# Kernel optimization log

Measured on AMD Instinct MI355X. Metric: run time of the kernel, lower is better.

Reference implementation:

```python
import jax, jax.numpy as jnp
import numpy as np

EPS = 1e-5
B, N = 16, 131072

def _bn(x, g, b, m, v):
    # x: [C, N]; inference-mode batchnorm with given stats
    return g[:, None] * (x - m[:, None]) * jax.lax.rsqrt(v[:, None] + EPS) + b[:, None]

def _make_npts():
    base = N // B
    offs = np.linspace(-2048, 2048, B).astype(np.int64)
    npts = np.full(B, base, dtype=np.int64) + offs
    npts[-1] += N - npts.sum()
    assert npts.sum() == N and (npts > 0).all()
    return npts

def setup_inputs() -> dict:
    key = jax.random.key(0)
    ks = jax.random.split(key, 16)
    d = {}
    d["x"] = jax.random.normal(ks[0], (3, N), jnp.float32)
    d["npts"] = jnp.asarray(_make_npts(), jnp.int32)
    def w(k, o, i):
        return jax.random.normal(k, (o, i), jnp.float32) * (1.0 / np.sqrt(i))
    def bnp(k, c):
        k1, k2, k3, k4 = jax.random.split(k, 4)
        return (1.0 + 0.1 * jax.random.normal(k1, (c,), jnp.float32),
                0.1 * jax.random.normal(k2, (c,), jnp.float32),
                0.1 * jax.random.normal(k3, (c,), jnp.float32),
                0.5 + jax.random.uniform(k4, (c,), jnp.float32))
    d["W1"] = w(ks[1], 128, 3);   d["b1"] = jnp.zeros(128, jnp.float32)
    d["g1"], d["be1"], d["m1"], d["v1"] = bnp(ks[2], 128)
    d["W2"] = w(ks[3], 256, 128); d["b2"] = jnp.zeros(256, jnp.float32)
    d["g2"], d["be2"], d["m2"], d["v2"] = bnp(ks[4], 256)
    d["W3"] = w(ks[5], 512, 512); d["b3"] = jnp.zeros(512, jnp.float32)
    d["g3"], d["be3"], d["m3"], d["v3"] = bnp(ks[6], 512)
    d["W4"] = w(ks[7], 1024, 512); d["b4"] = jnp.zeros(1024, jnp.float32)
    d["g4"], d["be4"], d["m4"], d["v4"] = bnp(ks[8], 1024)
    return d

def reference(x, npts,
              W1, b1, g1, be1, m1, v1,
              W2, b2, g2, be2, m2, v2,
              W3, b3, g3, be3, m3, v3,
              W4, b4, g4, be4, m4, v4):
    # segment ids for the ragged point->cloud mapping (replaces torch.split loops)
    seg = jnp.repeat(jnp.arange(B, dtype=jnp.int32), npts, total_repeat_length=N)  # [N]
    h = jax.nn.relu(_bn(W1 @ x + b1[:, None], g1, be1, m1, v1))        # [128, N]
    f = _bn(W2 @ h + b2[:, None], g2, be2, m2, v2)                      # [256, N]
    g = jax.ops.segment_max(f.T, seg, num_segments=B)                   # [B, 256]
    gs = g[seg].T                                                       # [256, N] broadcast back
    xc = jnp.concatenate([gs, f], axis=0)                               # [512, N]
    h3 = jax.nn.relu(_bn(W3 @ xc + b3[:, None], g3, be3, m3, v3))       # [512, N]
    h4 = _bn(W4 @ h3 + b4[:, None], g4, be4, m4, v4)                    # [1024, N]
    v = jax.ops.segment_max(h4.T, seg, num_segments=B)                  # [B, 1024]
    return v
```

## Files before the change

### kernel.cpp

```cpp
#include <hip/hip_runtime.h>
#include <hip/hip_bf16.h>
#include <stdint.h>

#define NTOT 131072
#define NSEG 16
#define EPSV 1e-5f

typedef __attribute__((ext_vector_type(8))) short bf16x8;
typedef __attribute__((ext_vector_type(4))) float f32x4;

struct Args {
  const float* x; const int* npts;
  const float *W1,*b1,*g1,*be1,*m1,*v1;
  const float *W2,*b2,*g2,*be2,*m2,*v2;
  const float *W3,*b3,*g3,*be3,*m3,*v3;
  const float *W4,*b4,*g4,*be4,*m4,*v4;
  int* offs;
  float *a1,*c1,*a2,*c2,*a3,*c3,*a4,*c4;
  unsigned int *gkeys,*vkeys;
  unsigned short *w2b;
  unsigned short *w3p;
  unsigned short *w4p;
  unsigned short *fbufp;
  unsigned short *h3p;
  float* cseg;
  float* out;
};

__device__ inline unsigned int f2key(float f){ unsigned u=__float_as_uint(f); return (u&0x80000000u)? ~u : (u|0x80000000u); }
__device__ inline float key2f(unsigned k){ unsigned u=(k&0x80000000u)? (k^0x80000000u) : ~k; return __uint_as_float(u); }
__device__ inline unsigned short f2bf(float f){ __hip_bfloat16 h=__float2bfloat16(f); return *(unsigned short*)&h; }

__device__ inline void gl16(const void* g, void* l){
  __builtin_amdgcn_global_load_lds((const __attribute__((address_space(1))) unsigned int*)g,
                                   (__attribute__((address_space(3))) unsigned int*)l, 16, 0, 0);
}

__global__ void k_setup(Args A){
  int tid = threadIdx.x;
  if (tid==0){ int s=0; A.offs[0]=0; for (int i=0;i<NSEG;i++){ s+=A.npts[i]; A.offs[i+1]=s; } }
  for (int c=tid;c<128;c+=256){ float a=A.g1[c]*rsqrtf(A.v1[c]+EPSV); A.a1[c]=a; A.c1[c]=A.be1[c]+a*(A.b1[c]-A.m1[c]); }
  for (int c=tid;c<256;c+=256){ float a=A.g2[c]*rsqrtf(A.v2[c]+EPSV); A.a2[c]=a; A.c2[c]=A.be2[c]+a*(A.b2[c]-A.m2[c]); }
  for (int c=tid;c<512;c+=256){ float a=A.g3[c]*rsqrtf(A.v3[c]+EPSV); A.a3[c]=a; A.c3[c]=A.be3[c]+a*(A.b3[c]-A.m3[c]); }
  for (int c=tid;c<1024;c+=256){ float a=A.g4[c]*rsqrtf(A.v4[c]+EPSV); A.a4[c]=a; A.c4[c]=A.be4[c]+a*(A.b4[c]-A.m4[c]); }
  for (int i=tid;i<NSEG*256;i+=256)  A.gkeys[i]=0u;
  for (int i=tid;i<NSEG*1024;i+=256) A.vkeys[i]=0u;
}

__global__ void k_conv(Args A){
  const int n1=256*128;
  const int n2=131072;
  const int n3=524288;
  for (int i = blockIdx.x*256+threadIdx.x; i < n1+n2+n3; i += gridDim.x*256){
    if (i<n1) A.w2b[i]=f2bf(A.W2[i]);
    else if (i<n1+n2){
      int o=i-n1; int j=o&7, cr=(o>>3)&127, kgg=(o>>10)&31, mt=o>>15;
      A.w3p[o]=f2bf(A.W3[(size_t)(mt*128+cr)*512 + 256 + kgg*8 + j]);
    } else {
      int o=i-n1-n2; int j=o&7, cr=(o>>3)&127, kgg=(o>>10)&63, mt=o>>16;
      A.w4p[o]=f2bf(A.W4[(size_t)(mt*128+cr)*512 + kgg*8 + j]);
    }
  }
}

__global__ __launch_bounds__(256) void k_l12(Args A){
  __shared__ float w1s[384], a1s[128], c1s[128], a2s[256], c2s[256];
  __shared__ float xs[3][64];
  __shared__ int offs_s[NSEG+1], segp[64];
  __shared__ unsigned short hs[16*64*8];
  int tid=threadIdx.x, pt0=blockIdx.x*64;
  for (int i=tid;i<384;i+=256) w1s[i]=A.W1[i];
  if (tid<128){ a1s[tid]=A.a1[tid]; c1s[tid]=A.c1[tid]; }
  a2s[tid]=A.a2[tid]; c2s[tid]=A.c2[tid];
  if (tid<=NSEG) offs_s[tid]=A.offs[tid];
  if (tid<64){ xs[0][tid]=A.x[pt0+tid]; xs[1][tid]=A.x[NTOT+pt0+tid]; xs[2][tid]=A.x[2*NTOT+pt0+tid]; }
  __syncthreads();
  if (tid<64){ int gp=pt0+tid, s=0; while (gp>=offs_s[s+1]) s++; segp[tid]=s; }
  for (int pair=tid; pair<1024; pair+=256){
    int pt=pair&63, kc=pair>>6;
    float x0=xs[0][pt], x1=xs[1][pt], x2=xs[2][pt];
    unsigned short us[8];
    #pragma unroll
    for (int j=0;j<8;j++){
      int cin=kc*8+j;
      float v = fmaf(w1s[cin*3],x0, fmaf(w1s[cin*3+1],x1, w1s[cin*3+2]*x2));
      v = fmaxf(fmaf(a1s[cin],v,c1s[cin]), 0.f);
      us[j]=f2bf(v);
    }
    uint4 pk;
    pk.x=(unsigned)us[0]|((unsigned)us[1]<<16); pk.y=(unsigned)us[2]|((unsigned)us[3]<<16);
    pk.z=(unsigned)us[4]|((unsigned)us[5]<<16); pk.w=(unsigned)us[6]|((unsigned)us[7]<<16);
    *(uint4*)(&hs[(kc*64+pt)*8]) = pk;
  }
  __syncthreads();
  int lane=tid&63, wv=tid>>6, quad=lane>>4, l16=lane&15;
  int m0=wv*64;
  f32x4 acc[4][4];
  for (int a=0;a<4;a++)
    for (int b=0;b<4;b++)
      acc[a][b]=(f32x4){0.f,0.f,0.f,0.f};
  #pragma unroll
  for (int ks=0; ks<4; ++ks){
    bf16x8 bfr[4];
    #pragma unroll
    for (int nt=0; nt<4; ++nt) bfr[nt]=*(bf16x8*)(&hs[((ks*4+quad)*64 + nt*16 + l16)*8]);
    #pragma unroll
    for (int mt=0; mt<4; ++mt){
      bf16x8 afr = *(const bf16x8*)(&A.w2b[(m0+mt*16+l16)*128 + ks*32 + quad*8]);
      #pragma unroll
      for (int nt=0; nt<4; ++nt)
        acc[mt][nt]=__builtin_amdgcn_mfma_f32_16x16x32_bf16(afr, bfr[nt], acc[mt][nt], 0,0,0);
    }
  }
  bool uni = (segp[0]==segp[63]); int seg0=segp[0];
  size_t tb = (size_t)(blockIdx.x>>1)*32768;
  int prelb = (blockIdx.x&1)*64;
  #pragma unroll
  for (int mt=0;mt<4;++mt){
    int cout0=m0+mt*16+quad*4;
    int kg=cout0>>3, sub=cout0&7;
    float fv[4][4];
    #pragma unroll
    for (int nt=0;nt<4;++nt)
      #pragma unroll
      for (int r=0;r<4;++r)
        fv[nt][r]=fmaf(a2s[cout0+r], acc[mt][nt][r], c2s[cout0+r]);
    #pragma unroll
    for (int nt=0;nt<4;++nt){
      int ptl=nt*16+l16;
      uint2 pk;
      pk.x=(unsigned)f2bf(fv[nt][0])|((unsigned)f2bf(fv[nt][1])<<16);
      pk.y=(unsigned)f2bf(fv[nt][2])|((unsigned)f2bf(fv[nt][3])<<16);
      *(uint2*)&A.fbufp[tb + (size_t)((kg*128 + prelb + ptl)*8 + sub)] = pk;
    }
    #pragma unroll
    for (int r=0;r<4;++r){
      if (uni){
        float mv=fmaxf(fmaxf(fv[0][r],fv[1][r]),fmaxf(fv[2][r],fv[3][r]));
        #pragma unroll
        for (int off=8;off>=1;off>>=1) mv=fmaxf(mv, __shfl_xor(mv,off));
        if (l16==0) atomicMax(&A.gkeys[seg0*256+cout0+r], f2key(mv));
      } else {
        #pragma unroll
        for (int nt=0;nt<4;++nt)
          atomicMax(&A.gkeys[segp[nt*16+l16]*256+cout0+r], f2key(fv[nt][r]));
      }
    }
  }
}

__global__ void k_cseg(Args A){
  int seg = blockIdx.x>>1; int cout = (blockIdx.x&1)*256 + threadIdx.x;
  __shared__ float gs[256];
  gs[threadIdx.x] = key2f(A.gkeys[seg*256+threadIdx.x]);
  __syncthreads();
  const float* wrow = A.W3 + (size_t)cout*512;
  float s=0.f;
  #pragma unroll 8
  for (int k=0;k<256;k++) s = fmaf(wrow[k], gs[k], s);
  A.cseg[seg*512+cout]=s;
}

__global__ __launch_bounds__(256,4) void k_l3(Args A){
  __shared__ unsigned short sA[8192], sB[8192];
  __shared__ int offs_s[NSEG+1];
  int bid=blockIdx.x, xcd=bid&7, idx=bid>>3;
  int mtile=idx&3, ntile=xcd*128+(idx>>2);
  int tid=threadIdx.x, lane=tid&63, wv=tid>>6, quad=lane>>4, l16=lane&15;
  int mq=wv&1, nq=wv>>1;
  const char* wbase=(const char*)A.w3p   + (size_t)mtile*65536;
  const char* bbase=(const char*)A.fbufp + (size_t)ntile*65536;
  if (tid<=NSEG) offs_s[tid]=A.offs[tid];
  f32x4 acc[4][4];
  for (int a=0;a<4;a++)
    for (int b=0;b<4;b++)
      acc[a][b]=(f32x4){0.f,0.f,0.f,0.f};
  for (int s=0;s<4;++s){
    const char* srcA = wbase + s*16384;
    const char* srcB = bbase + s*16384;
    #pragma unroll
    for (int i=0;i<4;++i){
      gl16(srcA + wv*4096 + i*1024 + lane*16, (char*)sA + wv*4096 + i*1024);
      gl16(srcB + wv*4096 + i*1024 + lane*16, (char*)sB + wv*4096 + i*1024);
    }
    __syncthreads();
    #pragma unroll
    for (int ks=0;ks<2;++ks){
      bf16x8 bb[4], afr[4];
      #pragma unroll
      for (int nt=0;nt<4;++nt) bb[nt]=*(const bf16x8*)(&sB[((ks*4+quad)*128 + nq*64 + nt*16 + l16)*8]);
      #pragma unroll
      for (int mt=0;mt<4;++mt) afr[mt]=*(const bf16x8*)(&sA[((ks*4+quad)*128 + mq*64 + mt*16 + l16)*8]);
      #pragma unroll
      for (int mt=0;mt<4;++mt)
        #pragma unroll
        for (int nt=0;nt<4;++nt)
          acc[mt][nt]=__builtin_amdgcn_mfma_f32_16x16x32_bf16(afr[mt], bb[nt], acc[mt][nt], 0,0,0);
    }
    __syncthreads();
  }
  int pt0 = ntile*128 + nq*64;
  int sBeg=0; while (pt0 >= offs_s[sBeg+1]) sBeg++;
  int sEnd=sBeg; while (pt0+63 >= offs_s[sEnd+1]) sEnd++;
  bool uni=(sBeg==sEnd);
  int segl[4];
  if (!uni){
    #pragma unroll
    for (int nt=0;nt<4;++nt){ int gp=pt0+nt*16+l16, ss=sBeg; while (gp>=offs_s[ss+1]) ss++; segl[nt]=ss; }
  }
  size_t hb = (size_t)ntile*65536;
  #pragma unroll
  for (int mt=0;mt<4;++mt){
    int cout0=mtile*128 + mq*64 + mt*16 + quad*4;
    int kg=cout0>>3, sub=cout0&7;
    float sa[4],sc[4],csr[4];
    #pragma unroll
    for (int r=0;r<4;++r){ sa[r]=A.a3[cout0+r]; sc[r]=A.c3[cout0+r]; }
    if (uni){
      #pragma unroll
      for (int r=0;r<4;++r) csr[r]=A.cseg[sBeg*512+cout0+r];
    }
    #pragma unroll
    for (int nt=0;nt<4;++nt){
      int prel=nq*64+nt*16+l16;
      unsigned short us[4];
      #pragma unroll
      for (int r=0;r<4;++r){
        float cv = uni? csr[r] : A.cseg[segl[nt]*512+cout0+r];
        float hv = fmaxf(fmaf(sa[r], acc[mt][nt][r]+cv, sc[r]), 0.f);
        us[r]=f2bf(hv);
      }
      uint2 pk;
      pk.x=(unsigned)us[0]|((unsigned)us[1]<<16);
      pk.y=(unsigned)us[2]|((unsigned)us[3]<<16);
      *(uint2*)&A.h3p[hb + (size_t)((kg*128+prel)*8+sub)] = pk;
    }
  }
}

__global__ __launch_bounds__(256,4) void k_l4(Args A){
  __shared__ unsigned short sA[8192], sB[8192];
  __shared__ int offs_s[NSEG+1];
  int bid=blockIdx.x, xcd=bid&7, idx=bid>>3;
  int mtile=idx&7, ntile=xcd*128+(idx>>3);
  int tid=threadIdx.x, lane=tid&63, wv=tid>>6, quad=lane>>4, l16=lane&15;
  int mq=wv&1, nq=wv>>1;
  const char* wbase=(const char*)A.w4p + (size_t)mtile*131072;
  const char* bbase=(const char*)A.h3p + (size_t)ntile*131072;
  if (tid<=NSEG) offs_s[tid]=A.offs[tid];
  f32x4 acc[4][4];
  for (int a=0;a<4;a++)
    for (int b=0;b<4;b++)
      acc[a][b]=(f32x4){0.f,0.f,0.f,0.f};
  for (int s=0;s<8;++s){
    const char* srcA = wbase + s*16384;
    const char* srcB = bbase + s*16384;
    #pragma unroll
    for (int i=0;i<4;++i){
      gl16(srcA + wv*4096 + i*1024 + lane*16, (char*)sA + wv*4096 + i*1024);
      gl16(srcB + wv*4096 + i*1024 + lane*16, (char*)sB + wv*4096 + i*1024);
    }
    __syncthreads();
    #pragma unroll
    for (int ks=0;ks<2;++ks){
      bf16x8 bb[4], afr[4];
      #pragma unroll
      for (int nt=0;nt<4;++nt) bb[nt]=*(const bf16x8*)(&sB[((ks*4+quad)*128 + nq*64 + nt*16 + l16)*8]);
      #pragma unroll
      for (int mt=0;mt<4;++mt) afr[mt]=*(const bf16x8*)(&sA[((ks*4+quad)*128 + mq*64 + mt*16 + l16)*8]);
      #pragma unroll
      for (int mt=0;mt<4;++mt)
        #pragma unroll
        for (int nt=0;nt<4;++nt)
          acc[mt][nt]=__builtin_amdgcn_mfma_f32_16x16x32_bf16(afr[mt], bb[nt], acc[mt][nt], 0,0,0);
    }
    __syncthreads();
  }
  int pt0 = ntile*128 + nq*64;
  int sBeg=0; while (pt0 >= offs_s[sBeg+1]) sBeg++;
  int sEnd=sBeg; while (pt0+63 >= offs_s[sEnd+1]) sEnd++;
  bool uni=(sBeg==sEnd);
  int segl[4];
  if (!uni){
    #pragma unroll
    for (int nt=0;nt<4;++nt){ int gp=pt0+nt*16+l16, ss=sBeg; while (gp>=offs_s[ss+1]) ss++; segl[nt]=ss; }
  }
  #pragma unroll
  for (int mt=0;mt<4;++mt){
    int cout0=mtile*128 + mq*64 + mt*16 + quad*4;
    #pragma unroll
    for (int r=0;r<4;++r){
      int cout=cout0+r;
      float sa=A.a4[cout], sc=A.c4[cout];
      float mv=-3.4e38f;
      #pragma unroll
      for (int nt=0;nt<4;++nt){
        float fv=fmaf(sa, acc[mt][nt][r], sc);
        if (uni) mv=fmaxf(mv,fv);
        else atomicMax(&A.vkeys[segl[nt]*1024+cout], f2key(fv));
      }
      if (uni){
        #pragma unroll
        for (int off=8;off>=1;off>>=1) mv=fmaxf(mv, __shfl_xor(mv,off));
        if (l16==0) atomicMax(&A.vkeys[sBeg*1024+cout], f2key(mv));
      }
    }
  }
}

__global__ void k_final(Args A){
  int i=blockIdx.x*256+threadIdx.x;
  if (i<NSEG*1024) A.out[i]=key2f(A.vkeys[i]);
}

extern "C" void kernel_launch(void* const* d_in, const int* in_sizes, int n_in,
                              void* d_out, int out_size, void* d_ws, size_t ws_size,
                              hipStream_t stream){
  Args A;
  A.x  =(const float*)d_in[0];  A.npts=(const int*)d_in[1];
  A.W1 =(const float*)d_in[2];  A.b1 =(const float*)d_in[3];
  A.g1 =(const float*)d_in[4];  A.be1=(const float*)d_in[5];
  A.m1 =(const float*)d_in[6];  A.v1 =(const float*)d_in[7];
  A.W2 =(const float*)d_in[8];  A.b2 =(const float*)d_in[9];
  A.g2 =(const float*)d_in[10]; A.be2=(const float*)d_in[11];
  A.m2 =(const float*)d_in[12]; A.v2 =(const float*)d_in[13];
  A.W3 =(const float*)d_in[14]; A.b3 =(const float*)d_in[15];
  A.g3 =(const float*)d_in[16]; A.be3=(const float*)d_in[17];
  A.m3 =(const float*)d_in[18]; A.v3 =(const float*)d_in[19];
  A.W4 =(const float*)d_in[20]; A.b4 =(const float*)d_in[21];
  A.g4 =(const float*)d_in[22]; A.be4=(const float*)d_in[23];
  A.m4 =(const float*)d_in[24]; A.v4 =(const float*)d_in[25];

  char* w=(char*)d_ws;
  auto alloc=[&](size_t b)->void*{ void* p=(void*)w; w += (b+255)&~(size_t)255; return p; };
  A.offs =(int*)alloc((NSEG+1)*4);
  A.a1=(float*)alloc(128*4);  A.c1=(float*)alloc(128*4);
  A.a2=(float*)alloc(256*4);  A.c2=(float*)alloc(256*4);
  A.a3=(float*)alloc(512*4);  A.c3=(float*)alloc(512*4);
  A.a4=(float*)alloc(1024*4); A.c4=(float*)alloc(1024*4);
  A.gkeys=(unsigned int*)alloc(NSEG*256*4);
  A.vkeys=(unsigned int*)alloc(NSEG*1024*4);
  A.cseg =(float*)alloc(NSEG*512*4);
  A.w2b=(unsigned short*)alloc(256*128*2);
  A.w3p=(unsigned short*)alloc(131072*2);
  A.w4p=(unsigned short*)alloc(524288*2);
  A.fbufp=(unsigned short*)alloc((size_t)1024*32768*2);
  A.h3p  =(unsigned short*)alloc((size_t)1024*65536*2);
  A.out=(float*)d_out;

  k_setup<<<dim3(1),dim3(256),0,stream>>>(A);
  k_conv <<<dim3(2688),dim3(256),0,stream>>>(A);
  k_l12  <<<dim3(NTOT/64),dim3(256),0,stream>>>(A);
  k_cseg <<<dim3(32),dim3(256),0,stream>>>(A);
  k_l3   <<<dim3(4096),dim3(256),0,stream>>>(A);
  k_l4   <<<dim3(8192),dim3(256),0,stream>>>(A);
  k_final<<<dim3(64),dim3(256),0,stream>>>(A);
}
```

Measured before the change: 604.2 us.

## Double-buffer LDS and make L3/L4 GEMM blocks persistent over four N-tiles

```diff
diff --git a/kernel.cpp b/kernel.cpp
--- a/kernel.cpp
+++ b/kernel.cpp
@@ -161,150 +161,192 @@
   A.cseg[seg*512+cout]=s;
 }
 
-__global__ __launch_bounds__(256,4) void k_l3(Args A){
-  __shared__ unsigned short sA[8192], sB[8192];
+__global__ __launch_bounds__(256,2) void k_l3(Args A){
+  __shared__ unsigned short sA[2][8192], sB[2][8192];
   __shared__ int offs_s[NSEG+1];
+  const int NST=16;
   int bid=blockIdx.x, xcd=bid&7, idx=bid>>3;
-  int mtile=idx&3, ntile=xcd*128+(idx>>2);
+  int mtile=idx&3, nq4=idx>>2;
+  int nbase=(xcd*32+nq4)*4;
   int tid=threadIdx.x, lane=tid&63, wv=tid>>6, quad=lane>>4, l16=lane&15;
   int mq=wv&1, nq=wv>>1;
-  const char* wbase=(const char*)A.w3p   + (size_t)mtile*65536;
-  const char* bbase=(const char*)A.fbufp + (size_t)ntile*65536;
+  const char* wbase=(const char*)A.w3p + (size_t)mtile*65536;
+  const char* bbase0=(const char*)A.fbufp;
   if (tid<=NSEG) offs_s[tid]=A.offs[tid];
   f32x4 acc[4][4];
   for (int a=0;a<4;a++)
     for (int b=0;b<4;b++)
       acc[a][b]=(f32x4){0.f,0.f,0.f,0.f};
-  for (int s=0;s<4;++s){
+
+  auto stage=[&](int buf,int ntile,int s){
     const char* srcA = wbase + s*16384;
-    const char* srcB = bbase + s*16384;
-    #pragma unroll
-    for (int i=0;i<4;++i){
-      gl16(srcA + wv*4096 + i*1024 + lane*16, (char*)sA + wv*4096 + i*1024);
-      gl16(srcB + wv*4096 + i*1024 + lane*16, (char*)sB + wv*4096 + i*1024);
+    const char* srcB = bbase0 + (size_t)ntile*65536 + s*16384;
+    char* dA=(char*)&sA[buf][0]; char* dB=(char*)&sB[buf][0];
+    #pragma unroll
+    for(int i=0;i<4;++i){
+      gl16(srcA + wv*4096 + i*1024 + lane*16, dA + wv*4096 + i*1024);
+      gl16(srcB + wv*4096 + i*1024 + lane*16, dB + wv*4096 + i*1024);
+    }
+  };
+
+  stage(0, nbase, 0);
+  __syncthreads();
+  for (int g=0; g<NST; ++g){
+    int buf=g&1, ntile=nbase+(g>>2), s=g&3;
+    bf16x8 afr[2][4], bbv[2][4];
+    #pragma unroll
+    for (int ks=0;ks<2;++ks){
+      #pragma unroll
+      for (int mt=0;mt<4;++mt) afr[ks][mt]=*(const bf16x8*)(&sA[buf][((ks*4+quad)*128 + mq*64 + mt*16 + l16)*8]);
+      #pragma unroll
+      for (int nt=0;nt<4;++nt) bbv[ks][nt]=*(const bf16x8*)(&sB[buf][((ks*4+quad)*128 + nq*64 + nt*16 + l16)*8]);
+    }
+    __builtin_amdgcn_sched_barrier(0);
+    if (g+1<NST) stage((g+1)&1, nbase+((g+1)>>2), (g+1)&3);
+    __builtin_amdgcn_sched_barrier(0);
+    __builtin_amdgcn_s_setprio(1);
+    #pragma unroll
+    for (int ks=0;ks<2;++ks)
+      #pragma unroll
+      for (int mt=0;mt<4;++mt)
+        #pragma unroll
+        for (int nt=0;nt<4;++nt)
+          acc[mt][nt]=__builtin_amdgcn_mfma_f32_16x16x32_bf16(afr[ks][mt], bbv[ks][nt], acc[mt][nt], 0,0,0);
+    __builtin_amdgcn_s_setprio(0);
+    if (s==3){
+      int pt0 = ntile*128 + nq*64;
+      int sBeg=0; while (pt0 >= offs_s[sBeg+1]) sBeg++;
+      int sEnd=sBeg; while (pt0+63 >= offs_s[sEnd+1]) sEnd++;
+      bool uni=(sBeg==sEnd);
+      int segl[4];
+      if (!uni){
+        #pragma unroll
+        for (int nt=0;nt<4;++nt){ int gp=pt0+nt*16+l16, ss=sBeg; while (gp>=offs_s[ss+1]) ss++; segl[nt]=ss; }
+      }
+      size_t hb = (size_t)ntile*65536;
+      #pragma unroll
+      for (int mt=0;mt<4;++mt){
+        int cout0=mtile*128 + mq*64 + mt*16 + quad*4;
+        int kg=cout0>>3, sub=cout0&7;
+        float sa[4],sc[4],csr[4];
+        #pragma unroll
+        for (int r=0;r<4;++r){ sa[r]=A.a3[cout0+r]; sc[r]=A.c3[cout0+r]; }
+        if (uni){
+          #pragma unroll
+          for (int r=0;r<4;++r) csr[r]=A.cseg[sBeg*512+cout0+r];
+        }
+        #pragma unroll
+        for (int nt=0;nt<4;++nt){
+          int prel=nq*64+nt*16+l16;
+          unsigned short us[4];
+          #pragma unroll
+          for (int r=0;r<4;++r){
+            float cv = uni? csr[r] : A.cseg[segl[nt]*512+cout0+r];
+            float hv = fmaxf(fmaf(sa[r], acc[mt][nt][r]+cv, sc[r]), 0.f);
+            us[r]=f2bf(hv);
+          }
+          uint2 pk;
+          pk.x=(unsigned)us[0]|((unsigned)us[1]<<16);
+          pk.y=(unsigned)us[2]|((unsigned)us[3]<<16);
+          *(uint2*)&A.h3p[hb + (size_t)((kg*128+prel)*8+sub)] = pk;
+        }
+      }
+      for (int a=0;a<4;a++)
+        for (int b=0;b<4;b++)
+          acc[a][b]=(f32x4){0.f,0.f,0.f,0.f};
     }
     __syncthreads();
-    #pragma unroll
-    for (int ks=0;ks<2;++ks){
-      bf16x8 bb[4], afr[4];
-      #pragma unroll
-      for (int nt=0;nt<4;++nt) bb[nt]=*(const bf16x8*)(&sB[((ks*4+quad)*128 + nq*64 + nt*16 + l16)*8]);
-      #pragma unroll
-      for (int mt=0;mt<4;++mt) afr[mt]=*(const bf16x8*)(&sA[((ks*4+quad)*128 + mq*64 + mt*16 + l16)*8]);
-      #pragma unroll
-      for (int mt=0;mt<4;++mt)
-        #pragma unroll
-        for (int nt=0;nt<4;++nt)
-          acc[mt][nt]=__builtin_amdgcn_mfma_f32_16x16x32_bf16(afr[mt], bb[nt], acc[mt][nt], 0,0,0);
-    }
-    __syncthreads();
-  }
-  int pt0 = ntile*128 + nq*64;
-  int sBeg=0; while (pt0 >= offs_s[sBeg+1]) sBeg++;
-  int sEnd=sBeg; while (pt0+63 >= offs_s[sEnd+1]) sEnd++;
-  bool uni=(sBeg==sEnd);
-  int segl[4];
-  if (!uni){
-    #pragma unroll
-    for (int nt=0;nt<4;++nt){ int gp=pt0+nt*16+l16, ss=sBeg; while (gp>=offs_s[ss+1]) ss++; segl[nt]=ss; }
-  }
-  size_t hb = (size_t)ntile*65536;
-  #pragma unroll
-  for (int mt=0;mt<4;++mt){
-    int cout0=mtile*128 + mq*64 + mt*16 + quad*4;
-    int kg=cout0>>3, sub=cout0&7;
-    float sa[4],sc[4],csr[4];
-    #pragma unroll
-    for (int r=0;r<4;++r){ sa[r]=A.a3[cout0+r]; sc[r]=A.c3[cout0+r]; }
-    if (uni){
-      #pragma unroll
-      for (int r=0;r<4;++r) csr[r]=A.cseg[sBeg*512+cout0+r];
-    }
-    #pragma unroll
-    for (int nt=0;nt<4;++nt){
-      int prel=nq*64+nt*16+l16;
-      unsigned short us[4];
-      #pragma unroll
-      for (int r=0;r<4;++r){
-        float cv = uni? csr[r] : A.cseg[segl[nt]*512+cout0+r];
-        float hv = fmaxf(fmaf(sa[r], acc[mt][nt][r]+cv, sc[r]), 0.f);
-        us[r]=f2bf(hv);
-      }
-      uint2 pk;
-      pk.x=(unsigned)us[0]|((unsigned)us[1]<<16);
-      pk.y=(unsigned)us[2]|((unsigned)us[3]<<16);
-      *(uint2*)&A.h3p[hb + (size_t)((kg*128+prel)*8+sub)] = pk;
-    }
-  }
-}
-
-__global__ __launch_bounds__(256,4) void k_l4(Args A){
-  __shared__ unsigned short sA[8192], sB[8192];
+  }
+}
+
+__global__ __launch_bounds__(256,2) void k_l4(Args A){
+  __shared__ unsigned short sA[2][8192], sB[2][8192];
   __shared__ int offs_s[NSEG+1];
+  const int NST=32;
   int bid=blockIdx.x, xcd=bid&7, idx=bid>>3;
-  int mtile=idx&7, ntile=xcd*128+(idx>>3);
+  int mtile=idx&7, nq4=idx>>3;
+  int nbase=(xcd*32+nq4)*4;
   int tid=threadIdx.x, lane=tid&63, wv=tid>>6, quad=lane>>4, l16=lane&15;
   int mq=wv&1, nq=wv>>1;
   const char* wbase=(const char*)A.w4p + (size_t)mtile*131072;
-  const char* bbase=(const char*)A.h3p + (size_t)ntile*131072;
+  const char* bbase0=(const char*)A.h3p;
   if (tid<=NSEG) offs_s[tid]=A.offs[tid];
   f32x4 acc[4][4];
   for (int a=0;a<4;a++)
     for (int b=0;b<4;b++)
       acc[a][b]=(f32x4){0.f,0.f,0.f,0.f};
-  for (int s=0;s<8;++s){
+
+  auto stage=[&](int buf,int ntile,int s){
     const char* srcA = wbase + s*16384;
-    const char* srcB = bbase + s*16384;
-    #pragma unroll
-    for (int i=0;i<4;++i){
-      gl16(srcA + wv*4096 + i*1024 + lane*16, (char*)sA + wv*4096 + i*1024);
-      gl16(srcB + wv*4096 + i*1024 + lane*16, (char*)sB + wv*4096 + i*1024);
+    const char* srcB = bbase0 + (size_t)ntile*131072 + s*16384;
+    char* dA=(char*)&sA[buf][0]; char* dB=(char*)&sB[buf][0];
+    #pragma unroll
+    for(int i=0;i<4;++i){
+      gl16(srcA + wv*4096 + i*1024 + lane*16, dA + wv*4096 + i*1024);
+      gl16(srcB + wv*4096 + i*1024 + lane*16, dB + wv*4096 + i*1024);
+    }
+  };
+
+  stage(0, nbase, 0);
+  __syncthreads();
+  for (int g=0; g<NST; ++g){
+    int buf=g&1, ntile=nbase+(g>>3), s=g&7;
+    bf16x8 afr[2][4], bbv[2][4];
+    #pragma unroll
+    for (int ks=0;ks<2;++ks){
+      #pragma unroll
+      for (int mt=0;mt<4;++mt) afr[ks][mt]=*(const bf16x8*)(&sA[buf][((ks*4+quad)*128 + mq*64 + mt*16 + l16)*8]);
+      #pragma unroll
+      for (int nt=0;nt<4;++nt) bbv[ks][nt]=*(const bf16x8*)(&sB[buf][((ks*4+quad)*128 + nq*64 + nt*16 + l16)*8]);
+    }
+    __builtin_amdgcn_sched_barrier(0);
+    if (g+1<NST) stage((g+1)&1, nbase+((g+1)>>3), (g+1)&7);
+    __builtin_amdgcn_sched_barrier(0);
+    __builtin_amdgcn_s_setprio(1);
+    #pragma unroll
+    for (int ks=0;ks<2;++ks)
+      #pragma unroll
+      for (int mt=0;mt<4;++mt)
+        #pragma unroll
+        for (int nt=0;nt<4;++nt)
+          acc[mt][nt]=__builtin_amdgcn_mfma_f32_16x16x32_bf16(afr[ks][mt], bbv[ks][nt], acc[mt][nt], 0,0,0);
+    __builtin_amdgcn_s_setprio(0);
+    if (s==7){
+      int pt0 = ntile*128 + nq*64;
+      int sBeg=0; while (pt0 >= offs_s[sBeg+1]) sBeg++;
+      int sEnd=sBeg; while (pt0+63 >= offs_s[sEnd+1]) sEnd++;
+      bool uni=(sBeg==sEnd);
+      int segl[4];
+      if (!uni){
+        #pragma unroll
+        for (int nt=0;nt<4;++nt){ int gp=pt0+nt*16+l16, ss=sBeg; while (gp>=offs_s[ss+1]) ss++; segl[nt]=ss; }
+      }
+      #pragma unroll
+      for (int mt=0;mt<4;++mt){
+        int cout0=mtile*128 + mq*64 + mt*16 + quad*4;
+        #pragma unroll
+        for (int r=0;r<4;++r){
+          int cout=cout0+r;
+          float sa=A.a4[cout], sc=A.c4[cout];
+          float mv=-3.4e38f;
+          #pragma unroll
+          for (int nt=0;nt<4;++nt){
+            float fv=fmaf(sa, acc[mt][nt][r], sc);
+            if (uni) mv=fmaxf(mv,fv);
+            else atomicMax(&A.vkeys[segl[nt]*1024+cout], f2key(fv));
+          }
+          if (uni){
+            #pragma unroll
+            for (int off=8;off>=1;off>>=1) mv=fmaxf(mv, __shfl_xor(mv,off));
+            if (l16==0) atomicMax(&A.vkeys[sBeg*1024+cout], f2key(mv));
+          }
+        }
+      }
+      for (int a=0;a<4;a++)
+        for (int b=0;b<4;b++)
+          acc[a][b]=(f32x4){0.f,0.f,0.f,0.f};
     }
     __syncthreads();
-    #pragma unroll
-    for (int ks=0;ks<2;++ks){
-      bf16x8 bb[4], afr[4];
-      #pragma unroll
-      for (int nt=0;nt<4;++nt) bb[nt]=*(const bf16x8*)(&sB[((ks*4+quad)*128 + nq*64 + nt*16 + l16)*8]);
-      #pragma unroll
-      for (int mt=0;mt<4;++mt) afr[mt]=*(const bf16x8*)(&sA[((ks*4+quad)*128 + mq*64 + mt*16 + l16)*8]);
-      #pragma unroll
-      for (int mt=0;mt<4;++mt)
-        #pragma unroll
-        for (int nt=0;nt<4;++nt)
-          acc[mt][nt]=__builtin_amdgcn_mfma_f32_16x16x32_bf16(afr[mt], bb[nt], acc[mt][nt], 0,0,0);
-    }
-    __syncthreads();
-  }
-  int pt0 = ntile*128 + nq*64;
-  int sBeg=0; while (pt0 >= offs_s[sBeg+1]) sBeg++;
-  int sEnd=sBeg; while (pt0+63 >= offs_s[sEnd+1]) sEnd++;
-  bool uni=(sBeg==sEnd);
-  int segl[4];
-  if (!uni){
-    #pragma unroll
-    for (int nt=0;nt<4;++nt){ int gp=pt0+nt*16+l16, ss=sBeg; while (gp>=offs_s[ss+1]) ss++; segl[nt]=ss; }
-  }
-  #pragma unroll
-  for (int mt=0;mt<4;++mt){
-    int cout0=mtile*128 + mq*64 + mt*16 + quad*4;
-    #pragma unroll
-    for (int r=0;r<4;++r){
-      int cout=cout0+r;
-      float sa=A.a4[cout], sc=A.c4[cout];
-      float mv=-3.4e38f;
-      #pragma unroll
-      for (int nt=0;nt<4;++nt){
-        float fv=fmaf(sa, acc[mt][nt][r], sc);
-        if (uni) mv=fmaxf(mv,fv);
-        else atomicMax(&A.vkeys[segl[nt]*1024+cout], f2key(fv));
-      }
-      if (uni){
-        #pragma unroll
-        for (int off=8;off>=1;off>>=1) mv=fmaxf(mv, __shfl_xor(mv,off));
-        if (l16==0) atomicMax(&A.vkeys[sBeg*1024+cout], f2key(mv));
-      }
-    }
   }
 }
 
@@ -352,7 +394,7 @@
   k_conv <<<dim3(2688),dim3(256),0,stream>>>(A);
   k_l12  <<<dim3(NTOT/64),dim3(256),0,stream>>>(A);
   k_cseg <<<dim3(32),dim3(256),0,stream>>>(A);
-  k_l3   <<<dim3(4096),dim3(256),0,stream>>>(A);
-  k_l4   <<<dim3(8192),dim3(256),0,stream>>>(A);
+  k_l3   <<<dim3(1024),dim3(256),0,stream>>>(A);
+  k_l4   <<<dim3(2048),dim3(256),0,stream>>>(A);
   k_final<<<dim3(64),dim3(256),0,stream>>>(A);
 }
```

After: 726.8 us. 20.3% more time.

## Fuse layer-3 and layer-4 GEMMs into one kernel keeping h3 in LDS

Applied to the files above, without the earlier changes.

```diff
diff --git a/kernel.cpp b/kernel.cpp
--- a/kernel.cpp
+++ b/kernel.cpp
@@ -22,7 +22,6 @@
   unsigned short *w3p;
   unsigned short *w4p;
   unsigned short *fbufp;
-  unsigned short *h3p;
   float* cseg;
   float* out;
 };
@@ -54,11 +53,11 @@
   for (int i = blockIdx.x*256+threadIdx.x; i < n1+n2+n3; i += gridDim.x*256){
     if (i<n1) A.w2b[i]=f2bf(A.W2[i]);
     else if (i<n1+n2){
-      int o=i-n1; int j=o&7, cr=(o>>3)&127, kgg=(o>>10)&31, mt=o>>15;
-      A.w3p[o]=f2bf(A.W3[(size_t)(mt*128+cr)*512 + 256 + kgg*8 + j]);
+      int o=i-n1; int j=o&7, cout=(o>>3)&255, kgrel=(o>>11)&3, ks=(o>>13)&7, cg=(o>>16)&1;
+      A.w3p[o]=f2bf(A.W3[(size_t)(cg*256+cout)*512 + 256 + ks*32 + kgrel*8 + j]);
     } else {
-      int o=i-n1-n2; int j=o&7, cr=(o>>3)&127, kgg=(o>>10)&63, mt=o>>16;
-      A.w4p[o]=f2bf(A.W4[(size_t)(mt*128+cr)*512 + kgg*8 + j]);
+      int o=i-n1-n2; int j=o&7, cout=(o>>3)&255, kgrel=(o>>11)&3, ks=(o>>13)&15, cg=(o>>17)&3;
+      A.w4p[o]=f2bf(A.W4[(size_t)(cg*256+cout)*512 + ks*32 + kgrel*8 + j]);
     }
   }
 }
@@ -113,8 +112,6 @@
     }
   }
   bool uni = (segp[0]==segp[63]); int seg0=segp[0];
-  size_t tb = (size_t)(blockIdx.x>>1)*32768;
-  int prelb = (blockIdx.x&1)*64;
   #pragma unroll
   for (int mt=0;mt<4;++mt){
     int cout0=m0+mt*16+quad*4;
@@ -131,7 +128,8 @@
       uint2 pk;
       pk.x=(unsigned)f2bf(fv[nt][0])|((unsigned)f2bf(fv[nt][1])<<16);
       pk.y=(unsigned)f2bf(fv[nt][2])|((unsigned)f2bf(fv[nt][3])<<16);
-      *(uint2*)&A.fbufp[tb + (size_t)((kg*128 + prelb + ptl)*8 + sub)] = pk;
+      size_t o = (size_t)(blockIdx.x*2 + (nt>>1))*8192 + (size_t)(kg*256 + ((nt&1)*16+l16)*8 + sub);
+      *(uint2*)&A.fbufp[o] = pk;
     }
     #pragma unroll
     for (int r=0;r<4;++r){
@@ -161,148 +159,157 @@
   A.cseg[seg*512+cout]=s;
 }
 
-__global__ __launch_bounds__(256,4) void k_l3(Args A){
-  __shared__ unsigned short sA[8192], sB[8192];
+__global__ __launch_bounds__(512,1) void k_l34(Args A){
+  __shared__ unsigned short h3s[65536];
+  __shared__ unsigned short fstg[8192];
   __shared__ int offs_s[NSEG+1];
-  int bid=blockIdx.x, xcd=bid&7, idx=bid>>3;
-  int mtile=idx&3, ntile=xcd*128+(idx>>2);
+  int blk=blockIdx.x;
   int tid=threadIdx.x, lane=tid&63, wv=tid>>6, quad=lane>>4, l16=lane&15;
-  int mq=wv&1, nq=wv>>1;
-  const char* wbase=(const char*)A.w3p   + (size_t)mtile*65536;
-  const char* bbase=(const char*)A.fbufp + (size_t)ntile*65536;
   if (tid<=NSEG) offs_s[tid]=A.offs[tid];
-  f32x4 acc[4][4];
-  for (int a=0;a<4;a++)
-    for (int b=0;b<4;b++)
-      acc[a][b]=(f32x4){0.f,0.f,0.f,0.f};
-  for (int s=0;s<4;++s){
-    const char* srcA = wbase + s*16384;
-    const char* srcB = bbase + s*16384;
-    #pragma unroll
-    for (int i=0;i<4;++i){
-      gl16(srcA + wv*4096 + i*1024 + lane*16, (char*)sA + wv*4096 + i*1024);
-      gl16(srcB + wv*4096 + i*1024 + lane*16, (char*)sB + wv*4096 + i*1024);
-    }
+  int c0=wv*64;
+
+  for (int chunk=0;chunk<4;++chunk){
+    const char* src=(const char*)A.fbufp + ((size_t)(blk*4+chunk))*16384;
+    gl16(src + wv*2048 + lane*16, (char*)fstg + wv*2048);
+    gl16(src + wv*2048 + 1024 + lane*16, (char*)fstg + wv*2048 + 1024);
     __syncthreads();
-    #pragma unroll
-    for (int ks=0;ks<2;++ks){
-      bf16x8 bb[4], afr[4];
-      #pragma unroll
-      for (int nt=0;nt<4;++nt) bb[nt]=*(const bf16x8*)(&sB[((ks*4+quad)*128 + nq*64 + nt*16 + l16)*8]);
-      #pragma unroll
-      for (int mt=0;mt<4;++mt) afr[mt]=*(const bf16x8*)(&sA[((ks*4+quad)*128 + mq*64 + mt*16 + l16)*8]);
+    f32x4 acc1[4][2];
+    #pragma unroll
+    for (int mt=0;mt<4;++mt)
+      #pragma unroll
+      for (int nt=0;nt<2;++nt)
+        acc1[mt][nt]=(f32x4){0.f,0.f,0.f,0.f};
+    #pragma unroll
+    for (int kk=0;kk<8;++kk){
+      bf16x8 bfr[2], afr[4];
+      #pragma unroll
+      for (int nt=0;nt<2;++nt)
+        bfr[nt]=*(const bf16x8*)(&fstg[((kk*4+quad)*32 + nt*16 + l16)*8]);
+      #pragma unroll
+      for (int mt=0;mt<4;++mt){
+        int cout=c0+mt*16+l16;
+        afr[mt]=*(const bf16x8*)(A.w3p + (size_t)((cout>>8)*65536 + kk*8192 + quad*2048 + (cout&255)*8));
+      }
+      __builtin_amdgcn_s_setprio(1);
       #pragma unroll
       for (int mt=0;mt<4;++mt)
         #pragma unroll
+        for (int nt=0;nt<2;++nt)
+          acc1[mt][nt]=__builtin_amdgcn_mfma_f32_16x16x32_bf16(afr[mt], bfr[nt], acc1[mt][nt], 0,0,0);
+      __builtin_amdgcn_s_setprio(0);
+    }
+    int pt0c = blk*128 + chunk*32;
+    int sBeg=0; while (pt0c >= offs_s[sBeg+1]) sBeg++;
+    int sEnd=sBeg; while (pt0c+31 >= offs_s[sEnd+1]) sEnd++;
+    bool uni=(sBeg==sEnd);
+    int segl[2];
+    if (!uni){
+      #pragma unroll
+      for (int nt=0;nt<2;++nt){ int gp=pt0c+nt*16+l16, ss=sBeg; while (gp>=offs_s[ss+1]) ss++; segl[nt]=ss; }
+    }
+    #pragma unroll
+    for (int mt=0;mt<4;++mt){
+      int cout0=c0+mt*16+quad*4;
+      int kg3=cout0>>3, sub3=cout0&7;
+      float sa[4],sc[4],csr[4];
+      #pragma unroll
+      for (int r=0;r<4;++r){ sa[r]=A.a3[cout0+r]; sc[r]=A.c3[cout0+r]; }
+      if (uni){
+        #pragma unroll
+        for (int r=0;r<4;++r) csr[r]=A.cseg[sBeg*512+cout0+r];
+      }
+      #pragma unroll
+      for (int nt=0;nt<2;++nt){
+        int ptt=chunk*32+nt*16+l16;
+        unsigned short us[4];
+        #pragma unroll
+        for (int r=0;r<4;++r){
+          float cv = uni? csr[r] : A.cseg[segl[nt]*512+cout0+r];
+          float hv = fmaxf(fmaf(sa[r], acc1[mt][nt][r]+cv, sc[r]), 0.f);
+          us[r]=f2bf(hv);
+        }
+        uint2 pk;
+        pk.x=(unsigned)us[0]|((unsigned)us[1]<<16);
+        pk.y=(unsigned)us[2]|((unsigned)us[3]<<16);
+        *(uint2*)&h3s[(size_t)((kg3*128+ptt)*8+sub3)] = pk;
+      }
+    }
+    __syncthreads();
+  }
+
+  for (int ci=0;ci<2;++ci){
+    int cc0=ci*512+c0;
+    f32x4 acc2[2][4][4];
+    #pragma unroll
+    for (int pi=0;pi<2;++pi)
+      #pragma unroll
+      for (int mt=0;mt<4;++mt)
+        #pragma unroll
         for (int nt=0;nt<4;++nt)
-          acc[mt][nt]=__builtin_amdgcn_mfma_f32_16x16x32_bf16(afr[mt], bb[nt], acc[mt][nt], 0,0,0);
-    }
-    __syncthreads();
-  }
-  int pt0 = ntile*128 + nq*64;
-  int sBeg=0; while (pt0 >= offs_s[sBeg+1]) sBeg++;
-  int sEnd=sBeg; while (pt0+63 >= offs_s[sEnd+1]) sEnd++;
-  bool uni=(sBeg==sEnd);
-  int segl[4];
-  if (!uni){
-    #pragma unroll
-    for (int nt=0;nt<4;++nt){ int gp=pt0+nt*16+l16, ss=sBeg; while (gp>=offs_s[ss+1]) ss++; segl[nt]=ss; }
-  }
-  size_t hb = (size_t)ntile*65536;
-  #pragma unroll
-  for (int mt=0;mt<4;++mt){
-    int cout0=mtile*128 + mq*64 + mt*16 + quad*4;
-    int kg=cout0>>3, sub=cout0&7;
-    float sa[4],sc[4],csr[4];
-    #pragma unroll
-    for (int r=0;r<4;++r){ sa[r]=A.a3[cout0+r]; sc[r]=A.c3[cout0+r]; }
-    if (uni){
-      #pragma unroll
-      for (int r=0;r<4;++r) csr[r]=A.cseg[sBeg*512+cout0+r];
-    }
-    #pragma unroll
-    for (int nt=0;nt<4;++nt){
-      int prel=nq*64+nt*16+l16;
-      unsigned short us[4];
-      #pragma unroll
-      for (int r=0;r<4;++r){
-        float cv = uni? csr[r] : A.cseg[segl[nt]*512+cout0+r];
-        float hv = fmaxf(fmaf(sa[r], acc[mt][nt][r]+cv, sc[r]), 0.f);
-        us[r]=f2bf(hv);
-      }
-      uint2 pk;
-      pk.x=(unsigned)us[0]|((unsigned)us[1]<<16);
-      pk.y=(unsigned)us[2]|((unsigned)us[3]<<16);
-      *(uint2*)&A.h3p[hb + (size_t)((kg*128+prel)*8+sub)] = pk;
-    }
-  }
-}
-
-__global__ __launch_bounds__(256,4) void k_l4(Args A){
-  __shared__ unsigned short sA[8192], sB[8192];
-  __shared__ int offs_s[NSEG+1];
-  int bid=blockIdx.x, xcd=bid&7, idx=bid>>3;
-  int mtile=idx&7, ntile=xcd*128+(idx>>3);
-  int tid=threadIdx.x, lane=tid&63, wv=tid>>6, quad=lane>>4, l16=lane&15;
-  int mq=wv&1, nq=wv>>1;
-  const char* wbase=(const char*)A.w4p + (size_t)mtile*131072;
-  const char* bbase=(const char*)A.h3p + (size_t)ntile*131072;
-  if (tid<=NSEG) offs_s[tid]=A.offs[tid];
-  f32x4 acc[4][4];
-  for (int a=0;a<4;a++)
-    for (int b=0;b<4;b++)
-      acc[a][b]=(f32x4){0.f,0.f,0.f,0.f};
-  for (int s=0;s<8;++s){
-    const char* srcA = wbase + s*16384;
-    const char* srcB = bbase + s*16384;
-    #pragma unroll
-    for (int i=0;i<4;++i){
-      gl16(srcA + wv*4096 + i*1024 + lane*16, (char*)sA + wv*4096 + i*1024);
-      gl16(srcB + wv*4096 + i*1024 + lane*16, (char*)sB + wv*4096 + i*1024);
-    }
-    __syncthreads();
-    #pragma unroll
-    for (int ks=0;ks<2;++ks){
-      bf16x8 bb[4], afr[4];
-      #pragma unroll
-      for (int nt=0;nt<4;++nt) bb[nt]=*(const bf16x8*)(&sB[((ks*4+quad)*128 + nq*64 + nt*16 + l16)*8]);
-      #pragma unroll
-      for (int mt=0;mt<4;++mt) afr[mt]=*(const bf16x8*)(&sA[((ks*4+quad)*128 + mq*64 + mt*16 + l16)*8]);
-      #pragma unroll
-      for (int mt=0;mt<4;++mt)
+          acc2[pi][mt][nt]=(f32x4){0.f,0.f,0.f,0.f};
+    bf16x8 aF[2][4];
+    #pragma unroll
+    for (int mt=0;mt<4;++mt){
+      int cout=cc0+mt*16+l16;
+      aF[0][mt]=*(const bf16x8*)(A.w4p + (size_t)((cout>>8)*131072 + quad*2048 + (cout&255)*8));
+    }
+    #pragma unroll
+    for (int kk=0;kk<16;++kk){
+      const int cb=kk&1, nb=cb^1;
+      if (kk<15){
+        #pragma unroll
+        for (int mt=0;mt<4;++mt){
+          int cout=cc0+mt*16+l16;
+          aF[nb][mt]=*(const bf16x8*)(A.w4p + (size_t)((cout>>8)*131072 + (kk+1)*8192 + quad*2048 + (cout&255)*8));
+        }
+      }
+      bf16x8 b2[2][4];
+      #pragma unroll
+      for (int pi=0;pi<2;++pi)
         #pragma unroll
         for (int nt=0;nt<4;++nt)
-          acc[mt][nt]=__builtin_amdgcn_mfma_f32_16x16x32_bf16(afr[mt], bb[nt], acc[mt][nt], 0,0,0);
-    }
-    __syncthreads();
-  }
-  int pt0 = ntile*128 + nq*64;
-  int sBeg=0; while (pt0 >= offs_s[sBeg+1]) sBeg++;
-  int sEnd=sBeg; while (pt0+63 >= offs_s[sEnd+1]) sEnd++;
-  bool uni=(sBeg==sEnd);
-  int segl[4];
-  if (!uni){
-    #pragma unroll
-    for (int nt=0;nt<4;++nt){ int gp=pt0+nt*16+l16, ss=sBeg; while (gp>=offs_s[ss+1]) ss++; segl[nt]=ss; }
-  }
-  #pragma unroll
-  for (int mt=0;mt<4;++mt){
-    int cout0=mtile*128 + mq*64 + mt*16 + quad*4;
-    #pragma unroll
-    for (int r=0;r<4;++r){
-      int cout=cout0+r;
-      float sa=A.a4[cout], sc=A.c4[cout];
-      float mv=-3.4e38f;
-      #pragma unroll
-      for (int nt=0;nt<4;++nt){
-        float fv=fmaf(sa, acc[mt][nt][r], sc);
-        if (uni) mv=fmaxf(mv,fv);
-        else atomicMax(&A.vkeys[segl[nt]*1024+cout], f2key(fv));
-      }
-      if (uni){
-        #pragma unroll
-        for (int off=8;off>=1;off>>=1) mv=fmaxf(mv, __shfl_xor(mv,off));
-        if (l16==0) atomicMax(&A.vkeys[sBeg*1024+cout], f2key(mv));
+          b2[pi][nt]=*(const bf16x8*)(&h3s[(size_t)(((kk*4+quad)*128 + pi*64 + nt*16 + l16)*8)]);
+      __builtin_amdgcn_s_setprio(1);
+      #pragma unroll
+      for (int pi=0;pi<2;++pi)
+        #pragma unroll
+        for (int mt=0;mt<4;++mt)
+          #pragma unroll
+          for (int nt=0;nt<4;++nt)
+            acc2[pi][mt][nt]=__builtin_amdgcn_mfma_f32_16x16x32_bf16(aF[cb][mt], b2[pi][nt], acc2[pi][mt][nt], 0,0,0);
+      __builtin_amdgcn_s_setprio(0);
+    }
+    #pragma unroll
+    for (int pi=0;pi<2;++pi){
+      int pt0=blk*128+pi*64;
+      int sBeg=0; while (pt0 >= offs_s[sBeg+1]) sBeg++;
+      int sEnd=sBeg; while (pt0+63 >= offs_s[sEnd+1]) sEnd++;
+      bool uni=(sBeg==sEnd);
+      int segl[4];
+      if (!uni){
+        #pragma unroll
+        for (int nt=0;nt<4;++nt){ int gp=pt0+nt*16+l16, ss=sBeg; while (gp>=offs_s[ss+1]) ss++; segl[nt]=ss; }
+      }
+      #pragma unroll
+      for (int mt=0;mt<4;++mt){
+        int cout0=cc0+mt*16+quad*4;
+        #pragma unroll
+        for (int r=0;r<4;++r){
+          int cout=cout0+r;
+          float sa=A.a4[cout], sc=A.c4[cout];
+          float mv=-3.4e38f;
+          #pragma unroll
+          for (int nt=0;nt<4;++nt){
+            float fv=fmaf(sa, acc2[pi][mt][nt][r], sc);
+            if (uni) mv=fmaxf(mv,fv);
+            else atomicMax(&A.vkeys[segl[nt]*1024+cout], f2key(fv));
+          }
+          if (uni){
+            #pragma unroll
+            for (int off=8;off>=1;off>>=1) mv=fmaxf(mv, __shfl_xor(mv,off));
+            if (l16==0) atomicMax(&A.vkeys[sBeg*1024+cout], f2key(mv));
+          }
+        }
       }
     }
   }
@@ -344,15 +351,13 @@
   A.w2b=(unsigned short*)alloc(256*128*2);
   A.w3p=(unsigned short*)alloc(131072*2);
   A.w4p=(unsigned short*)alloc(524288*2);
-  A.fbufp=(unsigned short*)alloc((size_t)1024*32768*2);
-  A.h3p  =(unsigned short*)alloc((size_t)1024*65536*2);
+  A.fbufp=(unsigned short*)alloc((size_t)4096*8192*2);
   A.out=(float*)d_out;
 
   k_setup<<<dim3(1),dim3(256),0,stream>>>(A);
   k_conv <<<dim3(2688),dim3(256),0,stream>>>(A);
   k_l12  <<<dim3(NTOT/64),dim3(256),0,stream>>>(A);
   k_cseg <<<dim3(32),dim3(256),0,stream>>>(A);
-  k_l3   <<<dim3(4096),dim3(256),0,stream>>>(A);
-  k_l4   <<<dim3(8192),dim3(256),0,stream>>>(A);
+  k_l34  <<<dim3(1024),dim3(512),0,stream>>>(A);
   k_final<<<dim3(64),dim3(256),0,stream>>>(A);
 }
```

Measured after the change: 933.3 us. 1.54x slower.

## Retile L3/L4 GEMMs to 256x64 blocks with weight fragments read directly from global

Applied to the files above, without the earlier changes.

```diff
diff --git a/kernel.cpp b/kernel.cpp
--- a/kernel.cpp
+++ b/kernel.cpp
@@ -162,35 +162,34 @@
 }
 
 __global__ __launch_bounds__(256,4) void k_l3(Args A){
-  __shared__ unsigned short sA[8192], sB[8192];
+  __shared__ unsigned short sB[4096];
   __shared__ int offs_s[NSEG+1];
-  int bid=blockIdx.x, xcd=bid&7, idx=bid>>3;
-  int mtile=idx&3, ntile=xcd*128+(idx>>2);
+  int bid=blockIdx.x, xcd=bid&7, j=bid>>3;
+  int Mt=j&1, ntile=xcd+8*(j>>1);
   int tid=threadIdx.x, lane=tid&63, wv=tid>>6, quad=lane>>4, l16=lane&15;
-  int mq=wv&1, nq=wv>>1;
-  const char* wbase=(const char*)A.w3p   + (size_t)mtile*65536;
-  const char* bbase=(const char*)A.fbufp + (size_t)ntile*65536;
+  int half=ntile&1, nt128=ntile>>1;
+  const char* bbase=(const char*)A.fbufp + (size_t)nt128*65536 + half*1024;
   if (tid<=NSEG) offs_s[tid]=A.offs[tid];
+  int coutw = Mt*256 + wv*64;
   f32x4 acc[4][4];
   for (int a=0;a<4;a++)
     for (int b=0;b<4;b++)
       acc[a][b]=(f32x4){0.f,0.f,0.f,0.f};
   for (int s=0;s<4;++s){
-    const char* srcA = wbase + s*16384;
-    const char* srcB = bbase + s*16384;
-    #pragma unroll
-    for (int i=0;i<4;++i){
-      gl16(srcA + wv*4096 + i*1024 + lane*16, (char*)sA + wv*4096 + i*1024);
-      gl16(srcB + wv*4096 + i*1024 + lane*16, (char*)sB + wv*4096 + i*1024);
-    }
+    const char* sb = bbase + (size_t)(s*8)*2048;
+    gl16(sb + (tid>>6)*2048 + (tid&63)*16, (char*)sB + tid*16);
+    gl16(sb + (4+(tid>>6))*2048 + (tid&63)*16, (char*)sB + 4096 + tid*16);
     __syncthreads();
     #pragma unroll
     for (int ks=0;ks<2;++ks){
       bf16x8 bb[4], afr[4];
       #pragma unroll
-      for (int nt=0;nt<4;++nt) bb[nt]=*(const bf16x8*)(&sB[((ks*4+quad)*128 + nq*64 + nt*16 + l16)*8]);
-      #pragma unroll
-      for (int mt=0;mt<4;++mt) afr[mt]=*(const bf16x8*)(&sA[((ks*4+quad)*128 + mq*64 + mt*16 + l16)*8]);
+      for (int nt=0;nt<4;++nt) bb[nt]=*(const bf16x8*)(&sB[((ks*4+quad)*64 + nt*16 + l16)*8]);
+      #pragma unroll
+      for (int mt=0;mt<4;++mt){
+        int cout = coutw + mt*16 + l16;
+        afr[mt]=*(const bf16x8*)(A.w3p + (size_t)((cout>>7)<<15) + ((s*8+ks*4+quad)<<10) + ((cout&127)<<3));
+      }
       #pragma unroll
       for (int mt=0;mt<4;++mt)
         #pragma unroll
@@ -199,7 +198,7 @@
     }
     __syncthreads();
   }
-  int pt0 = ntile*128 + nq*64;
+  int pt0 = ntile*64;
   int sBeg=0; while (pt0 >= offs_s[sBeg+1]) sBeg++;
   int sEnd=sBeg; while (pt0+63 >= offs_s[sEnd+1]) sEnd++;
   bool uni=(sBeg==sEnd);
@@ -208,10 +207,10 @@
     #pragma unroll
     for (int nt=0;nt<4;++nt){ int gp=pt0+nt*16+l16, ss=sBeg; while (gp>=offs_s[ss+1]) ss++; segl[nt]=ss; }
   }
-  size_t hb = (size_t)ntile*65536;
+  size_t hb = (size_t)nt128*65536;
   #pragma unroll
   for (int mt=0;mt<4;++mt){
-    int cout0=mtile*128 + mq*64 + mt*16 + quad*4;
+    int cout0=coutw + mt*16 + quad*4;
     int kg=cout0>>3, sub=cout0&7;
     float sa[4],sc[4],csr[4];
     #pragma unroll
@@ -222,7 +221,7 @@
     }
     #pragma unroll
     for (int nt=0;nt<4;++nt){
-      int prel=nq*64+nt*16+l16;
+      int prel=half*64 + nt*16+l16;
       unsigned short us[4];
       #pragma unroll
       for (int r=0;r<4;++r){
@@ -239,35 +238,34 @@
 }
 
 __global__ __launch_bounds__(256,4) void k_l4(Args A){
-  __shared__ unsigned short sA[8192], sB[8192];
+  __shared__ unsigned short sB[4096];
   __shared__ int offs_s[NSEG+1];
-  int bid=blockIdx.x, xcd=bid&7, idx=bid>>3;
-  int mtile=idx&7, ntile=xcd*128+(idx>>3);
+  int bid=blockIdx.x, xcd=bid&7, j=bid>>3;
+  int Mt=j&3, ntile=xcd+8*(j>>2);
   int tid=threadIdx.x, lane=tid&63, wv=tid>>6, quad=lane>>4, l16=lane&15;
-  int mq=wv&1, nq=wv>>1;
-  const char* wbase=(const char*)A.w4p + (size_t)mtile*131072;
-  const char* bbase=(const char*)A.h3p + (size_t)ntile*131072;
+  int half=ntile&1, nt128=ntile>>1;
+  const char* bbase=(const char*)A.h3p + (size_t)nt128*131072 + half*1024;
   if (tid<=NSEG) offs_s[tid]=A.offs[tid];
+  int coutw = Mt*256 + wv*64;
   f32x4 acc[4][4];
   for (int a=0;a<4;a++)
     for (int b=0;b<4;b++)
       acc[a][b]=(f32x4){0.f,0.f,0.f,0.f};
   for (int s=0;s<8;++s){
-    const char* srcA = wbase + s*16384;
-    const char* srcB = bbase + s*16384;
-    #pragma unroll
-    for (int i=0;i<4;++i){
-      gl16(srcA + wv*4096 + i*1024 + lane*16, (char*)sA + wv*4096 + i*1024);
-      gl16(srcB + wv*4096 + i*1024 + lane*16, (char*)sB + wv*4096 + i*1024);
-    }
+    const char* sb = bbase + (size_t)(s*8)*2048;
+    gl16(sb + (tid>>6)*2048 + (tid&63)*16, (char*)sB + tid*16);
+    gl16(sb + (4+(tid>>6))*2048 + (tid&63)*16, (char*)sB + 4096 + tid*16);
     __syncthreads();
     #pragma unroll
     for (int ks=0;ks<2;++ks){
       bf16x8 bb[4], afr[4];
       #pragma unroll
-      for (int nt=0;nt<4;++nt) bb[nt]=*(const bf16x8*)(&sB[((ks*4+quad)*128 + nq*64 + nt*16 + l16)*8]);
-      #pragma unroll
-      for (int mt=0;mt<4;++mt) afr[mt]=*(const bf16x8*)(&sA[((ks*4+quad)*128 + mq*64 + mt*16 + l16)*8]);
+      for (int nt=0;nt<4;++nt) bb[nt]=*(const bf16x8*)(&sB[((ks*4+quad)*64 + nt*16 + l16)*8]);
+      #pragma unroll
+      for (int mt=0;mt<4;++mt){
+        int cout = coutw + mt*16 + l16;
+        afr[mt]=*(const bf16x8*)(A.w4p + (size_t)((cout>>7)<<16) + ((s*8+ks*4+quad)<<10) + ((cout&127)<<3));
+      }
       #pragma unroll
       for (int mt=0;mt<4;++mt)
         #pragma unroll
@@ -276,7 +274,7 @@
     }
     __syncthreads();
   }
-  int pt0 = ntile*128 + nq*64;
+  int pt0 = ntile*64;
   int sBeg=0; while (pt0 >= offs_s[sBeg+1]) sBeg++;
   int sEnd=sBeg; while (pt0+63 >= offs_s[sEnd+1]) sEnd++;
   bool uni=(sBeg==sEnd);
@@ -287,7 +285,7 @@
   }
   #pragma unroll
   for (int mt=0;mt<4;++mt){
-    int cout0=mtile*128 + mq*64 + mt*16 + quad*4;
+    int cout0=coutw + mt*16 + quad*4;
     #pragma unroll
     for (int r=0;r<4;++r){
       int cout=cout0+r;
```

New measurement: 688.6 us. 14.0% more time.
